# Kernel tuning notes

Measured on AMD Instinct MI355X. Metric: run time of the kernel, lower is better.

Reference implementation:

```python
import jax, jax.numpy as jnp
import numpy as np

N_NODES = 100000
N_EDGES = 1600000
D_FEAT = 128
HIDDEN = 128
N_CLASSES = 10
N_GRAPHS = 512


def setup_inputs() -> dict:
    key = jax.random.key(0)
    ks = jax.random.split(key, 8)
    x = jax.random.normal(ks[0], (N_NODES, D_FEAT), dtype=jnp.float32)
    edge_index = jax.random.randint(ks[1], (2, N_EDGES), 0, N_NODES, dtype=jnp.int64)
    batch = jnp.sort(jax.random.randint(ks[2], (N_NODES,), 0, N_GRAPHS, dtype=jnp.int64))
    s = 1.0 / np.sqrt(D_FEAT)
    W1 = jax.random.normal(ks[3], (D_FEAT, HIDDEN), dtype=jnp.float32) * s
    W2 = jax.random.normal(ks[4], (HIDDEN, HIDDEN), dtype=jnp.float32) * s
    W3 = jax.random.normal(ks[5], (HIDDEN, HIDDEN), dtype=jnp.float32) * s
    Wl = jax.random.normal(ks[6], (HIDDEN, N_CLASSES), dtype=jnp.float32) * s
    return {
        'x': x, 'edge_index': edge_index, 'batch': batch,
        'W1': W1, 'b1': jnp.zeros((HIDDEN,), jnp.float32),
        'W2': W2, 'b2': jnp.zeros((HIDDEN,), jnp.float32),
        'W3': W3, 'b3': jnp.zeros((HIDDEN,), jnp.float32),
        'Wl': Wl, 'bl': jnp.zeros((N_CLASSES,), jnp.float32),
    }


def _gcn_norm(edge_index, n_nodes):
    # add self-loops + symmetric normalization (PyG GCNConv defaults)
    loop = jnp.arange(n_nodes, dtype=edge_index.dtype)
    src = jnp.concatenate([edge_index[0], loop])
    dst = jnp.concatenate([edge_index[1], loop])
    deg = jax.ops.segment_sum(jnp.ones_like(dst, jnp.float32), dst, num_segments=n_nodes)
    dinv = jnp.where(deg > 0, jax.lax.rsqrt(deg), 0.0)
    norm = dinv[src] * dinv[dst]  # [E+N]
    return src, dst, norm


def _gcn_conv(x, src, dst, norm, W, b, n_nodes):
    h = x @ W                                   # [N, H]
    msg = norm[:, None] * h[src]                # gather + scale, [E+N, H]
    out = jax.ops.segment_sum(msg, dst, num_segments=n_nodes)  # scatter-add
    return out + b


def reference(x, edge_index, batch, W1, b1, W2, b2, W3, b3, Wl, bl):
    n = x.shape[0]
    src, dst, norm = _gcn_norm(edge_index, n)
    h = jax.nn.relu(_gcn_conv(x, src, dst, norm, W1, b1, n))
    h = jax.nn.relu(_gcn_conv(h, src, dst, norm, W2, b2, n))
    h = _gcn_conv(h, src, dst, norm, W3, b3, n)
    # global mean pool over graphs
    sums = jax.ops.segment_sum(h, batch, num_segments=N_GRAPHS)        # [G, H]
    cnts = jax.ops.segment_sum(jnp.ones((n,), jnp.float32), batch, num_segments=N_GRAPHS)
    pooled = sums / jnp.maximum(cnts, 1.0)[:, None]
    # dropout is identity in eval mode
    return pooled @ Wl + bl                                            # [G, C]
```

## Files before the change

### kernel.cpp

```cpp
#include <hip/hip_runtime.h>
#include <cstdint>
#include <cstddef>

typedef _Float16 half8 __attribute__((ext_vector_type(8)));
typedef float    f32x4 __attribute__((ext_vector_type(4)));

#define NBLK 512
#define BSHIFT 8

static __device__ __forceinline__ float4 ld4(const float* p) {
    return *reinterpret_cast<const float4*>(p);
}

static __device__ __forceinline__ void ld8h(const _Float16* p, float* f) {
    half8 v = *reinterpret_cast<const half8*>(p);
#pragma unroll
    for (int k = 0; k < 8; ++k) f[k] = (float)v[k];
}


__global__ __launch_bounds__(256)
void binA_count(const int* __restrict__ dst, int* __restrict__ cntM,
                int e, int nb, int tile) {
    __shared__ int lc[512];
    const int t = threadIdx.x, j = blockIdx.x;
    lc[t] = 0; lc[t + 256] = 0;
    __syncthreads();
    const int lo = j * tile;
    const int hi = min(e, lo + tile);
    const int4* d4 = (const int4*)(dst + lo);
    const int n4 = (hi - lo) >> 2;
    for (int i = t; i < n4; i += 256) {
        int4 q = d4[i];
        atomicAdd(&lc[q.x >> BSHIFT], 1);
        atomicAdd(&lc[q.y >> BSHIFT], 1);
        atomicAdd(&lc[q.z >> BSHIFT], 1);
        atomicAdd(&lc[q.w >> BSHIFT], 1);
    }
    __syncthreads();
    for (int b = t; b < nb; b += 256) cntM[b * NBLK + j] = lc[b];
}

__global__ __launch_bounds__(256)
void scan1_kernel(const int* __restrict__ cnt, int* __restrict__ blockSums, int n) {
    __shared__ int ts[256];
    const int t = threadIdx.x;
    const int base = blockIdx.x * 1024 + t * 4;
    int s = 0;
    if (base + 3 < n) {
        int4 q = *reinterpret_cast<const int4*>(cnt + base);
        s = q.x + q.y + q.z + q.w;
    } else {
#pragma unroll
        for (int j = 0; j < 4; ++j) if (base + j < n) s += cnt[base + j];
    }
    ts[t] = s;
    __syncthreads();
    for (int off = 128; off > 0; off >>= 1) {
        if (t < off) ts[t] += ts[t + off];
        __syncthreads();
    }
    if (t == 0) blockSums[blockIdx.x] = ts[0];
}

__global__ __launch_bounds__(1024)
void scan_top_kernel(const int* __restrict__ blockSums, int* __restrict__ blockOff,
                     int* __restrict__ total, int nb) {
    __shared__ int ls[1024];
    const int t = threadIdx.x;
    ls[t] = (t < nb) ? blockSums[t] : 0;
    __syncthreads();
    for (int off = 1; off < 1024; off <<= 1) {
        int v = (t >= off) ? ls[t - off] : 0;
        __syncthreads();
        ls[t] += v;
        __syncthreads();
    }
    if (t < nb) blockOff[t] = (t == 0) ? 0 : ls[t - 1];
    if (t == 1023) total[0] = ls[1023];
}

__global__ __launch_bounds__(256)
void scan2_kernel(const int* __restrict__ cnt, const int* __restrict__ blockOff,
                  int* __restrict__ outp, int n) {
    __shared__ int ts[256];
    const int t = threadIdx.x;
    const int base = blockIdx.x * 1024 + t * 4;
    int v[4] = {0, 0, 0, 0};
    if (base + 3 < n) {
        int4 q = *reinterpret_cast<const int4*>(cnt + base);
        v[0] = q.x; v[1] = q.y; v[2] = q.z; v[3] = q.w;
    } else {
#pragma unroll
        for (int j = 0; j < 4; ++j) if (base + j < n) v[j] = cnt[base + j];
    }
    int s = v[0] + v[1] + v[2] + v[3];
    ts[t] = s;
    __syncthreads();
    for (int off = 1; off < 256; off <<= 1) {
        int x = (t >= off) ? ts[t - off] : 0;
        __syncthreads();
        ts[t] += x;
        __syncthreads();
    }
    int excl = blockOff[blockIdx.x] + ((t == 0) ? 0 : ts[t - 1]);
#pragma unroll
    for (int j = 0; j < 4; ++j) {
        if (base + j < n) outp[base + j] = excl;
        excl += v[j];
    }
}

__global__ __launch_bounds__(256)
void binA_place(const int* __restrict__ src, const int* __restrict__ dst,
                const int* __restrict__ offM, unsigned* __restrict__ staging,
                int e, int nb, int tile) {
    __shared__ int cur[512];
    const int t = threadIdx.x, j = blockIdx.x;
    for (int b = t; b < nb; b += 256) cur[b] = offM[b * NBLK + j];
    __syncthreads();
    const int lo = j * tile;
    const int hi = min(e, lo + tile);
    const int4* s4 = (const int4*)(src + lo);
    const int4* d4 = (const int4*)(dst + lo);
    const int n4 = (hi - lo) >> 2;
    for (int i = t; i < n4; i += 256) {
        int4 qs = s4[i];
        int4 qd = d4[i];
        int p0 = atomicAdd(&cur[qd.x >> BSHIFT], 1);
        staging[p0] = ((unsigned)qs.x << 8) | (unsigned)(qd.x & 255);
        int p1 = atomicAdd(&cur[qd.y >> BSHIFT], 1);
        staging[p1] = ((unsigned)qs.y << 8) | (unsigned)(qd.y & 255);
        int p2 = atomicAdd(&cur[qd.z >> BSHIFT], 1);
        staging[p2] = ((unsigned)qs.z << 8) | (unsigned)(qd.z & 255);
        int p3 = atomicAdd(&cur[qd.w >> BSHIFT], 1);
        staging[p3] = ((unsigned)qs.w << 8) | (unsigned)(qd.w & 255);
    }
}

__global__ __launch_bounds__(256)
void bucket_build(const unsigned* __restrict__ staging, const int* __restrict__ offM,
                  int* __restrict__ rowptr, float* __restrict__ dinv,
                  int* __restrict__ rec, int n, int nb, int e) {
    __shared__ int lc[256];
    __shared__ int ls[256];
    __shared__ int cur[256];
    const int b = blockIdx.x, t = threadIdx.x;
    const int base = offM[b * NBLK];
    const int end  = (b + 1 < nb) ? offM[(b + 1) * NBLK] : e;
    const int d0 = b << BSHIFT;
    const int R  = min(n - d0, 256);
    lc[t] = 0;
    __syncthreads();
    for (int i = base + t; i < end; i += 256) atomicAdd(&lc[staging[i] & 255u], 1);
    __syncthreads();
    const int deg = lc[t];
    ls[t] = deg;
    __syncthreads();
    for (int off = 1; off < 256; off <<= 1) {
        int v = (t >= off) ? ls[t - off] : 0;
        __syncthreads();
        ls[t] += v;
        __syncthreads();
    }
    int excl = (t == 0) ? 0 : ls[t - 1];
    if (t < R) {
        rowptr[d0 + t] = base + excl;
        dinv[d0 + t]   = rsqrtf((float)(deg + 1));
    }
    cur[t] = base + excl;
    if (b == nb - 1 && t == 0) rowptr[n] = e;
    __syncthreads();
    for (int i = base + t; i < end; i += 256) {
        unsigned q = staging[i];
        int pos = atomicAdd(&cur[q & 255u], 1);
        rec[pos] = (int)(q >> 8);
    }
}

template<int IN32>
__global__ __launch_bounds__(256)
void gemm_mfma_kernel(const void* __restrict__ Xv, const float* __restrict__ W,
                      _Float16* __restrict__ H16, int n) {
    __shared__ _Float16 Wt[128][136];
    __shared__ _Float16 Sw[4][16][136];

    const int t = threadIdx.x;
#pragma unroll
    for (int j = 0; j < 16; ++j) {
        int i4 = t + 256 * j;
        int k  = i4 >> 5;
        int c4 = (i4 & 31) * 4;
        float4 v = ld4(W + (size_t)i4 * 4);
        Wt[c4 + 0][k] = (_Float16)v.x;
        Wt[c4 + 1][k] = (_Float16)v.y;
        Wt[c4 + 2][k] = (_Float16)v.z;
        Wt[c4 + 3][k] = (_Float16)v.w;
    }
    __syncthreads();

    const int wave = t >> 6;
    const int l    = t & 63;
    const int lr   = l & 15;
    const int lk   = l >> 4;
    const int rowA = blockIdx.x * 64 + wave * 16 + lr;

    half8 a[4];
#pragma unroll
    for (int ks = 0; ks < 4; ++ks) {
#pragma unroll
        for (int j = 0; j < 8; ++j) a[ks][j] = (_Float16)0.f;
    }
    if (rowA < n) {
        if (IN32) {
            const float* X = (const float*)Xv;
#pragma unroll
            for (int ks = 0; ks < 4; ++ks) {
                const float* p = X + (size_t)rowA * 128 + ks * 32 + lk * 8;
                float4 f0 = ld4(p);
                float4 f1 = ld4(p + 4);
                a[ks][0] = (_Float16)f0.x; a[ks][1] = (_Float16)f0.y;
                a[ks][2] = (_Float16)f0.z; a[ks][3] = (_Float16)f0.w;
                a[ks][4] = (_Float16)f1.x; a[ks][5] = (_Float16)f1.y;
                a[ks][6] = (_Float16)f1.z; a[ks][7] = (_Float16)f1.w;
            }
        } else {
            const _Float16* X = (const _Float16*)Xv;
#pragma unroll
            for (int ks = 0; ks < 4; ++ks)
                a[ks] = *reinterpret_cast<const half8*>(X + (size_t)rowA * 128 + ks * 32 + lk * 8);
        }
    }

#pragma unroll
    for (int tt = 0; tt < 8; ++tt) {
        f32x4 acc = {0.f, 0.f, 0.f, 0.f};
#pragma unroll
        for (int ks = 0; ks < 4; ++ks) {
            half8 b = *reinterpret_cast<const half8*>(&Wt[tt * 16 + lr][ks * 32 + lk * 8]);
            acc = __builtin_amdgcn_mfma_f32_16x16x32_f16(a[ks], b, acc, 0, 0, 0);
        }
#pragma unroll
        for (int r = 0; r < 4; ++r)
            Sw[wave][lk * 4 + r][tt * 16 + lr] = (_Float16)acc[r];
    }
    __syncthreads();

#pragma unroll
    for (int j = 0; j < 4; ++j) {
        int chunk = l + 64 * j;
        int r  = chunk >> 4;
        int c8 = chunk & 15;
        int gr = blockIdx.x * 64 + wave * 16 + r;
        if (gr < n) {
            half8 v = *reinterpret_cast<const half8*>(&Sw[wave][r][c8 * 8]);
            *reinterpret_cast<half8*>(H16 + (size_t)gr * 128 + c8 * 8) = v;
        }
    }
}

__global__ __launch_bounds__(256)
void gather_kernel(const int* __restrict__ rowptr, const int* __restrict__ rec,
                   const float* __restrict__ dinv,
                   const _Float16* __restrict__ h16, const float* __restrict__ bias,
                   _Float16* __restrict__ outb, int n, int do_relu) {
    int gid  = blockIdx.x * blockDim.x + threadIdx.x;
    int node = gid >> 4;
    int lane = gid & 15;
    if (node >= n) return;

    int rs = rowptr[node];
    int re = rowptr[node + 1];
    float di = dinv[node];
    const int fo = lane * 8;

    float acc[8];
    {
        float f[8];
        ld8h(h16 + (size_t)node * 128 + fo, f);
        float c = di * di;
#pragma unroll
        for (int k = 0; k < 8; ++k) acc[k] = c * f[k];
    }

    for (int e0 = rs; e0 < re; e0 += 16) {
        int m = re - e0;
        if (m > 16) m = 16;
        int   sI = 0;
        float wI = 0.f;
        if (lane < m) {
            sI = rec[e0 + lane];
            wI = dinv[sI] * di;
        }
        int j = 0;
        for (; j + 3 < m; j += 4) {
            int   s0 = __shfl(sI, j,     16);
            float w0 = __shfl(wI, j,     16);
            int   s1 = __shfl(sI, j + 1, 16);
            float w1 = __shfl(wI, j + 1, 16);
            int   s2 = __shfl(sI, j + 2, 16);
            float w2 = __shfl(wI, j + 2, 16);
            int   s3 = __shfl(sI, j + 3, 16);
            float w3 = __shfl(wI, j + 3, 16);
            float f0[8], f1[8], f2[8], f3[8];
            ld8h(h16 + (size_t)s0 * 128 + fo, f0);
            ld8h(h16 + (size_t)s1 * 128 + fo, f1);
            ld8h(h16 + (size_t)s2 * 128 + fo, f2);
            ld8h(h16 + (size_t)s3 * 128 + fo, f3);
#pragma unroll
            for (int k = 0; k < 8; ++k) {
                acc[k] = fmaf(w0, f0[k], acc[k]);
                acc[k] = fmaf(w1, f1[k], acc[k]);
                acc[k] = fmaf(w2, f2[k], acc[k]);
                acc[k] = fmaf(w3, f3[k], acc[k]);
            }
        }
        for (; j < m; ++j) {
            int   s0 = __shfl(sI, j, 16);
            float w0 = __shfl(wI, j, 16);
            float f0[8];
            ld8h(h16 + (size_t)s0 * 128 + fo, f0);
#pragma unroll
            for (int k = 0; k < 8; ++k) acc[k] = fmaf(w0, f0[k], acc[k]);
        }
    }

    float4 b0 = ld4(bias + fo);
    float4 b1 = ld4(bias + fo + 4);
    acc[0] += b0.x; acc[1] += b0.y; acc[2] += b0.z; acc[3] += b0.w;
    acc[4] += b1.x; acc[5] += b1.y; acc[6] += b1.z; acc[7] += b1.w;
    if (do_relu) {
#pragma unroll
        for (int k = 0; k < 8; ++k) acc[k] = fmaxf(acc[k], 0.f);
    }
    half8 v;
#pragma unroll
    for (int k = 0; k < 8; ++k) v[k] = (_Float16)acc[k];
    *reinterpret_cast<half8*>(outb + (size_t)node * 128 + fo) = v;
}

__global__ __launch_bounds__(256)
void pool_final_kernel(const _Float16* __restrict__ h, const int* __restrict__ batch,
                       const float* __restrict__ Wl, const float* __restrict__ bl,
                       float* __restrict__ out, int n, int n_classes) {
    __shared__ f32x4 red[16][34];
    __shared__ float cpart[10][16];
    int g = blockIdx.x;
    int lo = 0, hi = n;
    while (lo < hi) { int mid = (lo + hi) >> 1; if (batch[mid] < g) lo = mid + 1; else hi = mid; }
    int start = lo;
    hi = n;
    while (lo < hi) { int mid = (lo + hi) >> 1; if (batch[mid] < g + 1) lo = mid + 1; else hi = mid; }
    int end = lo;

    const int t   = threadIdx.x;
    const int grp = t >> 4;
    const int ln  = t & 15;

    float acc[8] = {0.f, 0.f, 0.f, 0.f, 0.f, 0.f, 0.f, 0.f};
    for (int i = start + grp; i < end; i += 16) {
        float f[8];
        ld8h(h + (size_t)i * 128 + ln * 8, f);
#pragma unroll
        for (int k = 0; k < 8; ++k) acc[k] += f[k];
    }
    red[grp][ln * 2]     = (f32x4){acc[0], acc[1], acc[2], acc[3]};
    red[grp][ln * 2 + 1] = (f32x4){acc[4], acc[5], acc[6], acc[7]};
    __syncthreads();
#pragma unroll
    for (int off = 8; off > 0; off >>= 1) {
        if (grp < off) {
            red[grp][ln * 2]     += red[grp + off][ln * 2];
            red[grp][ln * 2 + 1] += red[grp + off][ln * 2 + 1];
        }
        __syncthreads();
    }
    if (t < n_classes * 16) {
        const int c = t >> 4;
        float p = 0.f;
#pragma unroll
        for (int k = 0; k < 8; ++k) {
            int kk = ln * 8 + k;
            p = fmaf(red[0][kk >> 2][kk & 3], Wl[kk * n_classes + c], p);
        }
        cpart[c][ln] = p;
    }
    __syncthreads();
    if (t < n_classes) {
        float s = 0.f;
#pragma unroll
        for (int k = 0; k < 16; ++k) s += cpart[t][k];
        float cnt = fmaxf((float)(end - start), 1.0f);
        out[g * n_classes + t] = s / cnt + bl[t];
    }
}

extern "C" void kernel_launch(void* const* d_in, const int* in_sizes, int n_in,
                              void* d_out, int out_size, void* d_ws, size_t ws_size,
                              hipStream_t stream) {
    const float* x     = (const float*)d_in[0];
    const int*   ei    = (const int*)d_in[1];
    const int*   batch = (const int*)d_in[2];
    const float* W1 = (const float*)d_in[3];
    const float* b1 = (const float*)d_in[4];
    const float* W2 = (const float*)d_in[5];
    const float* b2 = (const float*)d_in[6];
    const float* W3 = (const float*)d_in[7];
    const float* b3 = (const float*)d_in[8];
    const float* Wl = (const float*)d_in[9];
    const float* bl = (const float*)d_in[10];
    float* out = (float*)d_out;

    const int N = in_sizes[0] / 128;
    const int E = in_sizes[1] / 2;
    const int C = 10;
    const int G = out_size / C;

    const int* srcI = ei;
    const int* dstI = ei + E;

    const int NB   = (N + 255) >> BSHIFT;
    const int M    = NB * NBLK;
    const int TILE = (((E + NBLK - 1) / NBLK) + 3) & ~3;
    const int scanB = (M + 1023) / 1024;

    char* w = (char*)d_ws;
    size_t off = 0;
    auto alloc = [&](size_t bytes) -> void* {
        void* p = w + off;
        off = (off + bytes + 255) & ~(size_t)255;
        return p;
    };

    int*      rowptr    = (int*)alloc((size_t)(N + 1) * 4);
    float*    dinv      = (float*)alloc((size_t)N * 4);
    int*      rec       = (int*)alloc((size_t)E * 4);
    unsigned* staging   = (unsigned*)alloc((size_t)E * 4);
    int*      cntM      = (int*)alloc((size_t)M * 4);
    int*      offM      = (int*)alloc((size_t)M * 4);
    int*      blockSums = (int*)alloc((size_t)scanB * 4);
    int*      blockOff  = (int*)alloc((size_t)scanB * 4);
    int*      scrTotal  = (int*)alloc(256);
    _Float16* h16       = (_Float16*)alloc((size_t)N * 128 * 2);
    _Float16* act16     = (_Float16*)alloc((size_t)N * 128 * 2);

    binA_count<<<NBLK, 256, 0, stream>>>(dstI, cntM, E, NB, TILE);
    scan1_kernel<<<scanB, 256, 0, stream>>>(cntM, blockSums, M);
    scan_top_kernel<<<1, 1024, 0, stream>>>(blockSums, blockOff, scrTotal, scanB);
    scan2_kernel<<<scanB, 256, 0, stream>>>(cntM, blockOff, offM, M);
    binA_place<<<NBLK, 256, 0, stream>>>(srcI, dstI, offM, staging, E, NB, TILE);
    bucket_build<<<NB, 256, 0, stream>>>(staging, offM, rowptr, dinv, rec, N, NB, E);

    const int gemmBlocks = (N + 63) / 64;
    const int gathBlocks = (N * 16 + 255) / 256;

    gemm_mfma_kernel<1><<<gemmBlocks, 256, 0, stream>>>(x, W1, h16, N);
    gather_kernel<<<gathBlocks, 256, 0, stream>>>(rowptr, rec, dinv, h16, b1, act16, N, 1);
    gemm_mfma_kernel<0><<<gemmBlocks, 256, 0, stream>>>(act16, W2, h16, N);
    gather_kernel<<<gathBlocks, 256, 0, stream>>>(rowptr, rec, dinv, h16, b2, act16, N, 1);
    gemm_mfma_kernel<0><<<gemmBlocks, 256, 0, stream>>>(act16, W3, h16, N);
    gather_kernel<<<gathBlocks, 256, 0, stream>>>(rowptr, rec, dinv, h16, b3, act16, N, 0);

    pool_final_kernel<<<G, 256, 0, stream>>>(act16, batch, Wl, bl, out, N, C);
}
```

Before: 347.8 us.

## Slice features into XCD-local column blocks with per-slice work queues for gather

Stores the hidden feature matrices in a slice-major layout of 8 column slices of 16 halves each, so that each slice of all nodes (about 3.2 MB) can sit in one XCD's L2. The gather kernel reads the XCD id and pulls tiles of 128 nodes from an atomic work queue, starting with its own slice and moving on to the others, so most random neighbor reads hit the local L2. The GEMM writes, the layer inputs and the pooling are changed to match the new layout. In exchange, each edge's index and weight are now reloaded once per slice (8 times), and the queues add atomic and barrier overhead.

```diff
diff --git a/kernel.cpp b/kernel.cpp
--- a/kernel.cpp
+++ b/kernel.cpp
@@ -227,8 +227,11 @@
         } else {
             const _Float16* X = (const _Float16*)Xv;
 #pragma unroll
-            for (int ks = 0; ks < 4; ++ks)
-                a[ks] = *reinterpret_cast<const half8*>(X + (size_t)rowA * 128 + ks * 32 + lk * 8);
+            for (int ks = 0; ks < 4; ++ks) {
+                int sl = ks * 2 + (lk >> 1);
+                a[ks] = *reinterpret_cast<const half8*>(
+                    X + ((size_t)sl * n + rowA) * 16 + (lk & 1) * 8);
+            }
         }
     }
 
@@ -254,89 +257,89 @@
         int gr = blockIdx.x * 64 + wave * 16 + r;
         if (gr < n) {
             half8 v = *reinterpret_cast<const half8*>(&Sw[wave][r][c8 * 8]);
-            *reinterpret_cast<half8*>(H16 + (size_t)gr * 128 + c8 * 8) = v;
-        }
-    }
-}
-
-__global__ __launch_bounds__(256)
-void gather_kernel(const int* __restrict__ rowptr, const int* __restrict__ rec,
-                   const float* __restrict__ dinv,
-                   const _Float16* __restrict__ h16, const float* __restrict__ bias,
-                   _Float16* __restrict__ outb, int n, int do_relu) {
-    int gid  = blockIdx.x * blockDim.x + threadIdx.x;
-    int node = gid >> 4;
-    int lane = gid & 15;
-    if (node >= n) return;
-
-    int rs = rowptr[node];
-    int re = rowptr[node + 1];
-    float di = dinv[node];
-    const int fo = lane * 8;
-
-    float acc[8];
-    {
-        float f[8];
-        ld8h(h16 + (size_t)node * 128 + fo, f);
-        float c = di * di;
-#pragma unroll
-        for (int k = 0; k < 8; ++k) acc[k] = c * f[k];
-    }
-
-    for (int e0 = rs; e0 < re; e0 += 16) {
-        int m = re - e0;
-        if (m > 16) m = 16;
-        int   sI = 0;
-        float wI = 0.f;
-        if (lane < m) {
-            sI = rec[e0 + lane];
-            wI = dinv[sI] * di;
-        }
-        int j = 0;
-        for (; j + 3 < m; j += 4) {
-            int   s0 = __shfl(sI, j,     16);
-            float w0 = __shfl(wI, j,     16);
-            int   s1 = __shfl(sI, j + 1, 16);
-            float w1 = __shfl(wI, j + 1, 16);
-            int   s2 = __shfl(sI, j + 2, 16);
-            float w2 = __shfl(wI, j + 2, 16);
-            int   s3 = __shfl(sI, j + 3, 16);
-            float w3 = __shfl(wI, j + 3, 16);
-            float f0[8], f1[8], f2[8], f3[8];
-            ld8h(h16 + (size_t)s0 * 128 + fo, f0);
-            ld8h(h16 + (size_t)s1 * 128 + fo, f1);
-            ld8h(h16 + (size_t)s2 * 128 + fo, f2);
-            ld8h(h16 + (size_t)s3 * 128 + fo, f3);
-#pragma unroll
-            for (int k = 0; k < 8; ++k) {
-                acc[k] = fmaf(w0, f0[k], acc[k]);
-                acc[k] = fmaf(w1, f1[k], acc[k]);
-                acc[k] = fmaf(w2, f2[k], acc[k]);
-                acc[k] = fmaf(w3, f3[k], acc[k]);
+            *reinterpret_cast<half8*>(
+                H16 + ((size_t)(c8 >> 1) * n + gr) * 16 + (c8 & 1) * 8) = v;
+        }
+    }
+}
+
+__global__ __launch_bounds__(256)
+void gather_xcd_kernel(const int* __restrict__ rowptr, const int* __restrict__ rec,
+                       const float* __restrict__ dinv,
+                       const _Float16* __restrict__ h16, const float* __restrict__ bias,
+                       _Float16* __restrict__ outb, int* __restrict__ queues,
+                       int n, int ntiles, int do_relu) {
+    __shared__ int s_item;
+    int xcd;
+    asm volatile("s_getreg_b32 %0, hwreg(HW_REG_XCC_ID)" : "=s"(xcd));
+    xcd &= 7;
+    const int t  = threadIdx.x;
+    const int po = (t & 1) * 8;
+
+    for (int q = 0; q < 8; ++q) {
+        const int slice = (xcd + q) & 7;
+        const size_t sb = (size_t)slice * n;
+        const float4 b0 = ld4(bias + slice * 16 + po);
+        const float4 b1 = ld4(bias + slice * 16 + po + 4);
+        while (true) {
+            if (t == 0) s_item = atomicAdd(&queues[slice], 1);
+            __syncthreads();
+            const int item = s_item;
+            __syncthreads();
+            if (item >= ntiles) break;
+
+            const int node = item * 128 + (t >> 1);
+            if (node < n) {
+                const int rs = rowptr[node];
+                const int re = rowptr[node + 1];
+                const float di = dinv[node];
+
+                float acc[8];
+                {
+                    float f[8];
+                    ld8h(h16 + (sb + node) * 16 + po, f);
+                    float c = di * di;
+#pragma unroll
+                    for (int k = 0; k < 8; ++k) acc[k] = c * f[k];
+                }
+                int e = rs;
+                for (; e + 1 < re; e += 2) {
+                    int s0 = __builtin_nontemporal_load(rec + e);
+                    int s1 = __builtin_nontemporal_load(rec + e + 1);
+                    float w0 = dinv[s0] * di;
+                    float w1 = dinv[s1] * di;
+                    float f0[8], f1[8];
+                    ld8h(h16 + (sb + s0) * 16 + po, f0);
+                    ld8h(h16 + (sb + s1) * 16 + po, f1);
+#pragma unroll
+                    for (int k = 0; k < 8; ++k) {
+                        acc[k] = fmaf(w0, f0[k], acc[k]);
+                        acc[k] = fmaf(w1, f1[k], acc[k]);
+                    }
+                }
+                if (e < re) {
+                    int s0 = __builtin_nontemporal_load(rec + e);
+                    float w0 = dinv[s0] * di;
+                    float f0[8];
+                    ld8h(h16 + (sb + s0) * 16 + po, f0);
+#pragma unroll
+                    for (int k = 0; k < 8; ++k) acc[k] = fmaf(w0, f0[k], acc[k]);
+                }
+
+                acc[0] += b0.x; acc[1] += b0.y; acc[2] += b0.z; acc[3] += b0.w;
+                acc[4] += b1.x; acc[5] += b1.y; acc[6] += b1.z; acc[7] += b1.w;
+                if (do_relu) {
+#pragma unroll
+                    for (int k = 0; k < 8; ++k) acc[k] = fmaxf(acc[k], 0.f);
+                }
+                half8 v;
+#pragma unroll
+                for (int k = 0; k < 8; ++k) v[k] = (_Float16)acc[k];
+                __builtin_nontemporal_store(v,
+                    reinterpret_cast<half8*>(outb + (sb + node) * 16 + po));
             }
         }
-        for (; j < m; ++j) {
-            int   s0 = __shfl(sI, j, 16);
-            float w0 = __shfl(wI, j, 16);
-            float f0[8];
-            ld8h(h16 + (size_t)s0 * 128 + fo, f0);
-#pragma unroll
-            for (int k = 0; k < 8; ++k) acc[k] = fmaf(w0, f0[k], acc[k]);
-        }
-    }
-
-    float4 b0 = ld4(bias + fo);
-    float4 b1 = ld4(bias + fo + 4);
-    acc[0] += b0.x; acc[1] += b0.y; acc[2] += b0.z; acc[3] += b0.w;
-    acc[4] += b1.x; acc[5] += b1.y; acc[6] += b1.z; acc[7] += b1.w;
-    if (do_relu) {
-#pragma unroll
-        for (int k = 0; k < 8; ++k) acc[k] = fmaxf(acc[k], 0.f);
-    }
-    half8 v;
-#pragma unroll
-    for (int k = 0; k < 8; ++k) v[k] = (_Float16)acc[k];
-    *reinterpret_cast<half8*>(outb + (size_t)node * 128 + fo) = v;
+    }
 }
 
 __global__ __launch_bounds__(256)
@@ -360,7 +363,7 @@
     float acc[8] = {0.f, 0.f, 0.f, 0.f, 0.f, 0.f, 0.f, 0.f};
     for (int i = start + grp; i < end; i += 16) {
         float f[8];
-        ld8h(h + (size_t)i * 128 + ln * 8, f);
+        ld8h(h + ((size_t)(ln >> 1) * n + i) * 16 + (ln & 1) * 8, f);
 #pragma unroll
         for (int k = 0; k < 8; ++k) acc[k] += f[k];
     }
@@ -440,26 +443,32 @@
     int*      offM      = (int*)alloc((size_t)M * 4);
     int*      blockSums = (int*)alloc((size_t)scanB * 4);
     int*      blockOff  = (int*)alloc((size_t)scanB * 4);
-    int*      scrTotal  = (int*)alloc(256);
+    int*      queues    = (int*)alloc(3 * 8 * 4);
     _Float16* h16       = (_Float16*)alloc((size_t)N * 128 * 2);
     _Float16* act16     = (_Float16*)alloc((size_t)N * 128 * 2);
 
+    hipMemsetAsync(queues, 0, 3 * 8 * 4, stream);
+
     binA_count<<<NBLK, 256, 0, stream>>>(dstI, cntM, E, NB, TILE);
     scan1_kernel<<<scanB, 256, 0, stream>>>(cntM, blockSums, M);
-    scan_top_kernel<<<1, 1024, 0, stream>>>(blockSums, blockOff, scrTotal, scanB);
+    scan_top_kernel<<<1, 1024, 0, stream>>>(blockSums, blockOff, cntM + M - 1, scanB);
     scan2_kernel<<<scanB, 256, 0, stream>>>(cntM, blockOff, offM, M);
     binA_place<<<NBLK, 256, 0, stream>>>(srcI, dstI, offM, staging, E, NB, TILE);
     bucket_build<<<NB, 256, 0, stream>>>(staging, offM, rowptr, dinv, rec, N, NB, E);
 
     const int gemmBlocks = (N + 63) / 64;
-    const int gathBlocks = (N * 16 + 255) / 256;
+    const int ntiles     = (N + 127) / 128;
+    const int gathBlocks = 2048;
 
     gemm_mfma_kernel<1><<<gemmBlocks, 256, 0, stream>>>(x, W1, h16, N);
-    gather_kernel<<<gathBlocks, 256, 0, stream>>>(rowptr, rec, dinv, h16, b1, act16, N, 1);
+    gather_xcd_kernel<<<gathBlocks, 256, 0, stream>>>(rowptr, rec, dinv, h16, b1, act16,
+                                                      queues, N, ntiles, 1);
     gemm_mfma_kernel<0><<<gemmBlocks, 256, 0, stream>>>(act16, W2, h16, N);
-    gather_kernel<<<gathBlocks, 256, 0, stream>>>(rowptr, rec, dinv, h16, b2, act16, N, 1);
+    gather_xcd_kernel<<<gathBlocks, 256, 0, stream>>>(rowptr, rec, dinv, h16, b2, act16,
+                                                      queues + 8, N, ntiles, 1);
     gemm_mfma_kernel<0><<<gemmBlocks, 256, 0, stream>>>(act16, W3, h16, N);
-    gather_kernel<<<gathBlocks, 256, 0, stream>>>(rowptr, rec, dinv, h16, b3, act16, N, 0);
+    gather_xcd_kernel<<<gathBlocks, 256, 0, stream>>>(rowptr, rec, dinv, h16, b3, act16,
+                                                      queues + 16, N, ntiles, 0);
 
     pool_final_kernel<<<G, 256, 0, stream>>>(act16, batch, Wl, bl, out, N, C);
 }
```

Measured after the change: 1.312 ms. 277% more time.

## Split node features into two 64-column slabs for cache-friendlier gather

Applied to the files above, without the earlier changes.

Stores the fp16 feature matrices as two column slabs of 64 features each (slab-major), and has each gather block process one slab, using 8 lanes per node instead of 16. Adjacent blocks handle the two slabs of the same node tile. This halves the working set touched by random neighbour gathers at any moment, which may improve L2/MALL hit rates, but the edge list, rowptr and dinv are now read twice per node. GEMM and pooling kernels are updated to read and write the new layout.

```diff
diff --git a/kernel.cpp b/kernel.cpp
--- a/kernel.cpp
+++ b/kernel.cpp
@@ -227,8 +227,10 @@
         } else {
             const _Float16* X = (const _Float16*)Xv;
 #pragma unroll
-            for (int ks = 0; ks < 4; ++ks)
-                a[ks] = *reinterpret_cast<const half8*>(X + (size_t)rowA * 128 + ks * 32 + lk * 8);
+            for (int ks = 0; ks < 4; ++ks) {
+                a[ks] = *reinterpret_cast<const half8*>(
+                    X + ((size_t)(ks >> 1) * n + rowA) * 64 + (ks & 1) * 32 + lk * 8);
+            }
         }
     }
 
@@ -254,7 +256,8 @@
         int gr = blockIdx.x * 64 + wave * 16 + r;
         if (gr < n) {
             half8 v = *reinterpret_cast<const half8*>(&Sw[wave][r][c8 * 8]);
-            *reinterpret_cast<half8*>(H16 + (size_t)gr * 128 + c8 * 8) = v;
+            *reinterpret_cast<half8*>(
+                H16 + ((size_t)(c8 >> 3) * n + gr) * 64 + (c8 & 7) * 8) = v;
         }
     }
 }
@@ -264,28 +267,32 @@
                    const float* __restrict__ dinv,
                    const _Float16* __restrict__ h16, const float* __restrict__ bias,
                    _Float16* __restrict__ outb, int n, int do_relu) {
-    int gid  = blockIdx.x * blockDim.x + threadIdx.x;
-    int node = gid >> 4;
-    int lane = gid & 15;
+    const int slice = blockIdx.x & 1;
+    const int tile  = blockIdx.x >> 1;
+    const int t     = threadIdx.x;
+    const int node  = tile * 32 + (t >> 3);
+    const int lane  = t & 7;
+    const int fo    = lane * 8;
     if (node >= n) return;
+
+    const size_t sb = (size_t)slice * n;
 
     int rs = rowptr[node];
     int re = rowptr[node + 1];
     float di = dinv[node];
-    const int fo = lane * 8;
 
     float acc[8];
     {
         float f[8];
-        ld8h(h16 + (size_t)node * 128 + fo, f);
+        ld8h(h16 + (sb + node) * 64 + fo, f);
         float c = di * di;
 #pragma unroll
         for (int k = 0; k < 8; ++k) acc[k] = c * f[k];
     }
 
-    for (int e0 = rs; e0 < re; e0 += 16) {
+    for (int e0 = rs; e0 < re; e0 += 8) {
         int m = re - e0;
-        if (m > 16) m = 16;
+        if (m > 8) m = 8;
         int   sI = 0;
         float wI = 0.f;
         if (lane < m) {
@@ -294,19 +301,19 @@
         }
         int j = 0;
         for (; j + 3 < m; j += 4) {
-            int   s0 = __shfl(sI, j,     16);
-            float w0 = __shfl(wI, j,     16);
-            int   s1 = __shfl(sI, j + 1, 16);
-            float w1 = __shfl(wI, j + 1, 16);
-            int   s2 = __shfl(sI, j + 2, 16);
-            float w2 = __shfl(wI, j + 2, 16);
-            int   s3 = __shfl(sI, j + 3, 16);
-            float w3 = __shfl(wI, j + 3, 16);
+            int   s0 = __shfl(sI, j,     8);
+            float w0 = __shfl(wI, j,     8);
+            int   s1 = __shfl(sI, j + 1, 8);
+            float w1 = __shfl(wI, j + 1, 8);
+            int   s2 = __shfl(sI, j + 2, 8);
+            float w2 = __shfl(wI, j + 2, 8);
+            int   s3 = __shfl(sI, j + 3, 8);
+            float w3 = __shfl(wI, j + 3, 8);
             float f0[8], f1[8], f2[8], f3[8];
-            ld8h(h16 + (size_t)s0 * 128 + fo, f0);
-            ld8h(h16 + (size_t)s1 * 128 + fo, f1);
-            ld8h(h16 + (size_t)s2 * 128 + fo, f2);
-            ld8h(h16 + (size_t)s3 * 128 + fo, f3);
+            ld8h(h16 + (sb + s0) * 64 + fo, f0);
+            ld8h(h16 + (sb + s1) * 64 + fo, f1);
+            ld8h(h16 + (sb + s2) * 64 + fo, f2);
+            ld8h(h16 + (sb + s3) * 64 + fo, f3);
 #pragma unroll
             for (int k = 0; k < 8; ++k) {
                 acc[k] = fmaf(w0, f0[k], acc[k]);
@@ -316,17 +323,17 @@
             }
         }
         for (; j < m; ++j) {
-            int   s0 = __shfl(sI, j, 16);
-            float w0 = __shfl(wI, j, 16);
+            int   s0 = __shfl(sI, j, 8);
+            float w0 = __shfl(wI, j, 8);
             float f0[8];
-            ld8h(h16 + (size_t)s0 * 128 + fo, f0);
+            ld8h(h16 + (sb + s0) * 64 + fo, f0);
 #pragma unroll
             for (int k = 0; k < 8; ++k) acc[k] = fmaf(w0, f0[k], acc[k]);
         }
     }
 
-    float4 b0 = ld4(bias + fo);
-    float4 b1 = ld4(bias + fo + 4);
+    float4 b0 = ld4(bias + slice * 64 + fo);
+    float4 b1 = ld4(bias + slice * 64 + fo + 4);
     acc[0] += b0.x; acc[1] += b0.y; acc[2] += b0.z; acc[3] += b0.w;
     acc[4] += b1.x; acc[5] += b1.y; acc[6] += b1.z; acc[7] += b1.w;
     if (do_relu) {
@@ -336,7 +343,7 @@
     half8 v;
 #pragma unroll
     for (int k = 0; k < 8; ++k) v[k] = (_Float16)acc[k];
-    *reinterpret_cast<half8*>(outb + (size_t)node * 128 + fo) = v;
+    *reinterpret_cast<half8*>(outb + (sb + node) * 64 + fo) = v;
 }
 
 __global__ __launch_bounds__(256)
@@ -360,7 +367,7 @@
     float acc[8] = {0.f, 0.f, 0.f, 0.f, 0.f, 0.f, 0.f, 0.f};
     for (int i = start + grp; i < end; i += 16) {
         float f[8];
-        ld8h(h + (size_t)i * 128 + ln * 8, f);
+        ld8h(h + ((size_t)(ln >> 3) * n + i) * 64 + (ln & 7) * 8, f);
 #pragma unroll
         for (int k = 0; k < 8; ++k) acc[k] += f[k];
     }
@@ -452,7 +459,7 @@
     bucket_build<<<NB, 256, 0, stream>>>(staging, offM, rowptr, dinv, rec, N, NB, E);
 
     const int gemmBlocks = (N + 63) / 64;
-    const int gathBlocks = (N * 16 + 255) / 256;
+    const int gathBlocks = ((N + 31) / 32) * 2;
 
     gemm_mfma_kernel<1><<<gemmBlocks, 256, 0, stream>>>(x, W1, h16, N);
     gather_kernel<<<gathBlocks, 256, 0, stream>>>(rowptr, rec, dinv, h16, b1, act16, N, 1);
```

Result: no change. 346.6 us (-0.3%).
